# Kernel optimization log

Measured on AMD Instinct MI355X. Metric: run time of the kernel, lower is better.

## Reference

```python
import jax, jax.numpy as jnp
import numpy as np

MARGIN = 0.1
TEMPERATURE = 0.07


def _l2norm(x, eps=1e-12):
    # matches F.normalize(dim=-1): x / max(||x||, eps)
    n = jnp.sqrt(jnp.sum(x * x, axis=-1, keepdims=True))
    return x / jnp.maximum(n, eps)


def setup_inputs() -> dict:
    key = jax.random.key(0)
    k1, k2 = jax.random.split(key)
    N, D = 16384, 512
    return {
        "student_features": jax.random.normal(k1, (N, D), dtype=jnp.float32),
        "teacher_features": jax.random.normal(k2, (N, D), dtype=jnp.float32),
    }


def reference(student_features, teacher_features):
    s = _l2norm(student_features)
    t = _l2norm(teacher_features)
    logits = jnp.matmul(s, t.T) / TEMPERATURE  # [N, N]
    n = logits.shape[0]
    # targets = 2*I - 1 : +1 on diagonal, -1 off-diagonal
    targets = 2.0 * jnp.eye(n, dtype=logits.dtype) - 1.0
    loss = -jnp.sum(jax.nn.log_sigmoid(targets * logits + MARGIN)) / n
    return loss
```

## Files before the change

### kernel.cpp

```cpp
#include <hip/hip_runtime.h>
#include <stdint.h>

#define TEMPERATURE 0.07f
#define MARGIN 0.1f
#define D_DIM 512
#define BM 128
#define BN 256
#define QSCALE 32.0f
#define SCALE_BYTE 0x7A7A7A7A
#define KS_STRIDE 524288


typedef int v8i32 __attribute__((ext_vector_type(8)));
typedef int v4i32 __attribute__((ext_vector_type(4)));
typedef float f32x16 __attribute__((ext_vector_type(16)));

__device__ __forceinline__ float softplus(float x) {
    return fmaxf(x, 0.0f) + __logf(1.0f + __expf(-fabsf(x)));
}

__device__ __forceinline__ unsigned enc_fp4(float v) {
    const float ay = fabsf(v);
    int c = 0;
    c += ay > 0.25f;
    c += ay > 0.75f;
    c += ay > 1.25f;
    c += ay > 1.75f;
    c += ay > 2.5f;
    c += ay > 3.5f;
    c += ay > 5.0f;
    return (unsigned)c | ((__float_as_uint(v) >> 28) & 8u);
}

__global__ __launch_bounds__(256) void norm_quant_pack_kernel(
    const float* __restrict__ s_in, const float* __restrict__ t_in,
    unsigned char* __restrict__ sp, unsigned char* __restrict__ tp,
    float* __restrict__ corr) {
    const int row = blockIdx.x * 4 + (threadIdx.x >> 6);
    const int lane = threadIdx.x & 63;
    const float4* s4 = (const float4*)(s_in + (size_t)row * D_DIM);
    const float4* t4 = (const float4*)(t_in + (size_t)row * D_DIM);
    float4 a0 = s4[lane * 2], a1 = s4[lane * 2 + 1];
    float4 b0 = t4[lane * 2], b1 = t4[lane * 2 + 1];
    float ss = a0.x * a0.x + a0.y * a0.y + a0.z * a0.z + a0.w * a0.w +
               a1.x * a1.x + a1.y * a1.y + a1.z * a1.z + a1.w * a1.w;
    float tt = b0.x * b0.x + b0.y * b0.y + b0.z * b0.z + b0.w * b0.w +
               b1.x * b1.x + b1.y * b1.y + b1.z * b1.z + b1.w * b1.w;
    float st = a0.x * b0.x + a0.y * b0.y + a0.z * b0.z + a0.w * b0.w +
               a1.x * b1.x + a1.y * b1.y + a1.z * b1.z + a1.w * b1.w;
#pragma unroll
    for (int off = 32; off > 0; off >>= 1) {
        ss += __shfl_down(ss, off);
        tt += __shfl_down(tt, off);
        st += __shfl_down(st, off);
    }
    ss = __shfl(ss, 0);
    tt = __shfl(tt, 0);
    const float ns = fmaxf(sqrtf(ss), 1e-12f);
    const float nt = fmaxf(sqrtf(tt), 1e-12f);
    if (lane == 0) {
        const float l = st / (ns * nt) * (1.0f / TEMPERATURE);
        corr[row] = softplus(-l - MARGIN) - softplus(l - MARGIN);
    }
    const float is = QSCALE / ns, it = QSCALE / nt;
    const unsigned ws_ = enc_fp4(a0.x * is) | (enc_fp4(a0.y * is) << 4) |
                         (enc_fp4(a0.z * is) << 8) | (enc_fp4(a0.w * is) << 12) |
                         (enc_fp4(a1.x * is) << 16) | (enc_fp4(a1.y * is) << 20) |
                         (enc_fp4(a1.z * is) << 24) | (enc_fp4(a1.w * is) << 28);
    const unsigned wt_ = enc_fp4(b0.x * it) | (enc_fp4(b0.y * it) << 4) |
                         (enc_fp4(b0.z * it) << 8) | (enc_fp4(b0.w * it) << 12) |
                         (enc_fp4(b1.x * it) << 16) | (enc_fp4(b1.y * it) << 20) |
                         (enc_fp4(b1.z * it) << 24) | (enc_fp4(b1.w * it) << 28);
    const size_t goff = (size_t)(lane >> 3) * KS_STRIDE +
                        (size_t)(row >> 4) * 512 + ((lane >> 2) & 1) * 256 +
                        (row & 15) * 16 + (lane & 3) * 4;
    *(unsigned*)(sp + goff) = ws_;
    *(unsigned*)(tp + goff) = wt_;
}

__global__ __launch_bounds__(256, 2) void gemm_loss_kernel(
    const unsigned char* __restrict__ Sp, const unsigned char* __restrict__ Tp,
    float* __restrict__ partial) {
    __shared__ float wsums[4];

    const int tid = threadIdx.x;
    const int wave = tid >> 6;
    const int lane = tid & 63;
    const int wm = wave >> 1;
    const int wn = wave & 1;

    const int b = blockIdx.x;
    const int xcd = b & 7;
    const int slot = b >> 3;
    const int sidx = slot >> 6;
    const int within = slot & 63;
    const int st_ = sidx * 8 + xcd;
    const int tm = (st_ >> 4) * 16 + (within >> 2);
    const int tn_ = (st_ & 15) * 4 + (within & 3);

    const int fl4 =
        ((lane >> 4) & 1) * 512 + (lane >> 5) * 256 + (lane & 15) * 16;

    const unsigned char* Ab = Sp + (size_t)(tm * 4 + wm * 2) * 1024 + fl4;
    const unsigned char* Bb = Tp + (size_t)(tn_ * 8 + wn * 4) * 1024 + fl4;

    f32x16 acc[2][4];
#pragma unroll
    for (int pa = 0; pa < 2; ++pa)
#pragma unroll
        for (int pb = 0; pb < 4; ++pb)
#pragma unroll
            for (int r = 0; r < 16; ++r) acc[pa][pb][r] = 0.0f;

    v4i32 aF0[2], bF0[4], aF1[2], bF1[4];

    auto load_step = [&](v4i32(&aF)[2], v4i32(&bF)[4], int ks) {
        const size_t ko = (size_t)ks * KS_STRIDE;
#pragma unroll
        for (int pa = 0; pa < 2; ++pa)
            aF[pa] = *(const v4i32*)(Ab + ko + pa * 1024);
#pragma unroll
        for (int pb = 0; pb < 4; ++pb)
            bF[pb] = *(const v4i32*)(Bb + ko + pb * 1024);
    };
    auto mfma_step = [&](v4i32(&aF)[2], v4i32(&bF)[4]) {
        v8i32 aX[2];
#pragma unroll
        for (int pa = 0; pa < 2; ++pa)
            aX[pa] = __builtin_shufflevector(aF[pa], aF[pa], 0, 1, 2, 3, 0, 1,
                                             2, 3);
#pragma unroll
        for (int pb = 0; pb < 4; ++pb) {
            v8i32 bX = __builtin_shufflevector(bF[pb], bF[pb], 0, 1, 2, 3, 0,
                                               1, 2, 3);
#pragma unroll
            for (int pa = 0; pa < 2; ++pa)
                acc[pa][pb] = __builtin_amdgcn_mfma_scale_f32_32x32x64_f8f6f4(
                    aX[pa], bX, acc[pa][pb], 4 , 4 ,
                    0, SCALE_BYTE, 0, SCALE_BYTE);
        }
    };

    load_step(aF0, bF0, 0);
    load_step(aF1, bF1, 1);
#pragma unroll
    for (int ks = 0; ks < 8; ks += 2) {
        mfma_step(aF0, bF0);
        if (ks + 2 < 8) load_step(aF0, bF0, ks + 2);
        mfma_step(aF1, bF1);
        if (ks + 3 < 8) load_step(aF1, bF1, ks + 3);
    }

    const float C1 = (1.0f / TEMPERATURE) * 1.4426950408889634f;
    const float C2 = -MARGIN * 1.4426950408889634f;
    float ysum = 0.0f, asum = 0.0f, lsum = 0.0f;
#pragma unroll
    for (int pa = 0; pa < 2; ++pa)
#pragma unroll
        for (int pb = 0; pb < 4; ++pb) {
            float prod = 1.0f;
#pragma unroll
            for (int r = 0; r < 16; ++r) {
                const float y = fmaf(acc[pa][pb][r], C1, C2);
                ysum += y;
                const float ay = fabsf(y);
                asum += ay;
                prod = fmaf(prod, __builtin_amdgcn_exp2f(-ay), prod);
            }
            lsum += __builtin_amdgcn_logf(prod);
        }
    float total =
        fmaf(ysum + asum, 0.5f, lsum) * 0.6931471805599453f;
#pragma unroll
    for (int off = 32; off > 0; off >>= 1) total += __shfl_down(total, off);
    if (lane == 0) wsums[wave] = total;
    __syncthreads();
    if (tid == 0)
        partial[b] = wsums[0] + wsums[1] + wsums[2] + wsums[3];
}

__global__ __launch_bounds__(1024) void reduce_kernel(
    const float* __restrict__ partial, int nPartials,
    const float* __restrict__ corr, int nCorr, int N,
    float* __restrict__ out) {
    const float4* p4 = (const float4*)partial;
    const float4* c4 = (const float4*)corr;
    float sx = 0.0f, sy = 0.0f, sz = 0.0f, sw = 0.0f;
    for (int i = threadIdx.x; i < nPartials / 4; i += 1024) {
        float4 v = p4[i];
        sx += v.x; sy += v.y; sz += v.z; sw += v.w;
    }
    for (int i = threadIdx.x; i < nCorr / 4; i += 1024) {
        float4 v = c4[i];
        sx += v.x; sy += v.y; sz += v.z; sw += v.w;
    }
    float s = (sx + sy) + (sz + sw);
#pragma unroll
    for (int off = 32; off > 0; off >>= 1) s += __shfl_down(s, off);
    __shared__ float ws[16];
    const int wave = threadIdx.x >> 6;
    const int lane = threadIdx.x & 63;
    if (lane == 0) ws[wave] = s;
    __syncthreads();
    if (threadIdx.x == 0) {
        float t = 0.0f;
#pragma unroll
        for (int w = 0; w < 16; ++w) t += ws[w];
        out[0] = t / (float)N;
    }
}

extern "C" void kernel_launch(void* const* d_in, const int* in_sizes, int n_in,
                              void* d_out, int out_size, void* d_ws, size_t ws_size,
                              hipStream_t stream) {
    (void)n_in; (void)out_size; (void)ws_size;
    const float* s_in = (const float*)d_in[0];
    const float* t_in = (const float*)d_in[1];
    const int N = in_sizes[0] / D_DIM;

    unsigned char* sp = (unsigned char*)d_ws;
    unsigned char* tp = sp + (size_t)N * (D_DIM / 2);
    float* partial = (float*)(tp + (size_t)N * (D_DIM / 2));
    const int nPartials = (N / BM) * (N / BN);
    float* corr = partial + nPartials;

    norm_quant_pack_kernel<<<N / 4, 256, 0, stream>>>(s_in, t_in, sp, tp,
                                                      corr);
    gemm_loss_kernel<<<nPartials, 256, 0, stream>>>(sp, tp, partial);
    reduce_kernel<<<1, 1024, 0, stream>>>(partial, nPartials, corr, N, N,
                                          (float*)d_out);
}
```

Baseline: 182.6 us.

## Fuse final reduction into GEMM via atomics and coalesce packed-operand stores

The separate reduce kernel is removed: each GEMM block atomically adds its partial into one accumulator, and the last block, chosen by a ticket counter, writes the mean. The norm/quant kernel now handles 16 rows per block, stages the packed FP4 words in shared memory so global stores are contiguous, and atomically adds the diagonal correction. The GEMM drops the explicit double-buffered register prefetch in favour of a simple loop, raises the occupancy hint to 3 blocks, and leaves the upper half of the MFMA operands undefined instead of duplicated. The atomics add contention and make the summation order nondeterministic, and removing the manual prefetch may expose more load latency.

Measured after the change: 338.1 us. 85.2% more time.

```diff
diff --git a/kernel.cpp b/kernel.cpp
--- a/kernel.cpp
+++ b/kernel.cpp
@@ -32,12 +32,15 @@
     return (unsigned)c | ((__float_as_uint(v) >> 28) & 8u);
 }
 
-__global__ __launch_bounds__(256) void norm_quant_pack_kernel(
+__global__ __launch_bounds__(1024) void norm_quant_pack_kernel(
     const float* __restrict__ s_in, const float* __restrict__ t_in,
     unsigned char* __restrict__ sp, unsigned char* __restrict__ tp,
-    float* __restrict__ corr) {
-    const int row = blockIdx.x * 4 + (threadIdx.x >> 6);
+    float* __restrict__ accum) {
+    __shared__ unsigned pls[2048];
+    __shared__ float cshr[16];
+    const int wave = threadIdx.x >> 6;
     const int lane = threadIdx.x & 63;
+    const int row = blockIdx.x * 16 + wave;
     const float4* s4 = (const float4*)(s_in + (size_t)row * D_DIM);
     const float4* t4 = (const float4*)(t_in + (size_t)row * D_DIM);
     float4 a0 = s4[lane * 2], a1 = s4[lane * 2 + 1];
@@ -60,7 +63,7 @@
     const float nt = fmaxf(sqrtf(tt), 1e-12f);
     if (lane == 0) {
         const float l = st / (ns * nt) * (1.0f / TEMPERATURE);
-        corr[row] = softplus(-l - MARGIN) - softplus(l - MARGIN);
+        cshr[wave] = softplus(-l - MARGIN) - softplus(l - MARGIN);
     }
     const float is = QSCALE / ns, it = QSCALE / nt;
     const unsigned ws_ = enc_fp4(a0.x * is) | (enc_fp4(a0.y * is) << 4) |
@@ -71,16 +74,29 @@
                          (enc_fp4(b0.z * it) << 8) | (enc_fp4(b0.w * it) << 12) |
                          (enc_fp4(b1.x * it) << 16) | (enc_fp4(b1.y * it) << 20) |
                          (enc_fp4(b1.z * it) << 24) | (enc_fp4(b1.w * it) << 28);
-    const size_t goff = (size_t)(lane >> 3) * KS_STRIDE +
-                        (size_t)(row >> 4) * 512 + ((lane >> 2) & 1) * 256 +
-                        (row & 15) * 16 + (lane & 3) * 4;
-    *(unsigned*)(sp + goff) = ws_;
-    *(unsigned*)(tp + goff) = wt_;
-}
-
-__global__ __launch_bounds__(256, 2) void gemm_loss_kernel(
+    const int widx =
+        (lane >> 3) * 128 + ((lane >> 2) & 1) * 64 + wave * 4 + (lane & 3);
+    pls[widx] = ws_;
+    pls[1024 + widx] = wt_;
+    __syncthreads();
+    const int t = threadIdx.x;
+    const int ks = t >> 7, rem = t & 127;
+    const size_t goff = (size_t)ks * KS_STRIDE + (size_t)blockIdx.x * 512 +
+                        (size_t)rem * 4;
+    *(unsigned*)(sp + goff) = pls[t];
+    *(unsigned*)(tp + goff) = pls[1024 + t];
+    if (t == 0) {
+        float c = 0.0f;
+#pragma unroll
+        for (int w = 0; w < 16; ++w) c += cshr[w];
+        atomicAdd(accum, c);
+    }
+}
+
+__global__ __launch_bounds__(256, 3) void gemm_loss_kernel(
     const unsigned char* __restrict__ Sp, const unsigned char* __restrict__ Tp,
-    float* __restrict__ partial) {
+    float* __restrict__ accum, unsigned* __restrict__ ticket,
+    float* __restrict__ out, float invN) {
     __shared__ float wsums[4];
 
     const int tid = threadIdx.x;
@@ -112,43 +128,31 @@
 #pragma unroll
             for (int r = 0; r < 16; ++r) acc[pa][pb][r] = 0.0f;
 
-    v4i32 aF0[2], bF0[4], aF1[2], bF1[4];
-
-    auto load_step = [&](v4i32(&aF)[2], v4i32(&bF)[4], int ks) {
+#pragma unroll
+    for (int ks = 0; ks < 8; ++ks) {
         const size_t ko = (size_t)ks * KS_STRIDE;
+        v4i32 aF[2], bF[4];
 #pragma unroll
         for (int pa = 0; pa < 2; ++pa)
             aF[pa] = *(const v4i32*)(Ab + ko + pa * 1024);
 #pragma unroll
         for (int pb = 0; pb < 4; ++pb)
             bF[pb] = *(const v4i32*)(Bb + ko + pb * 1024);
-    };
-    auto mfma_step = [&](v4i32(&aF)[2], v4i32(&bF)[4]) {
         v8i32 aX[2];
 #pragma unroll
         for (int pa = 0; pa < 2; ++pa)
-            aX[pa] = __builtin_shufflevector(aF[pa], aF[pa], 0, 1, 2, 3, 0, 1,
-                                             2, 3);
+            aX[pa] = __builtin_shufflevector(aF[pa], aF[pa], 0, 1, 2, 3, -1,
+                                             -1, -1, -1);
 #pragma unroll
         for (int pb = 0; pb < 4; ++pb) {
-            v8i32 bX = __builtin_shufflevector(bF[pb], bF[pb], 0, 1, 2, 3, 0,
-                                               1, 2, 3);
+            v8i32 bX = __builtin_shufflevector(bF[pb], bF[pb], 0, 1, 2, 3, -1,
+                                               -1, -1, -1);
 #pragma unroll
             for (int pa = 0; pa < 2; ++pa)
                 acc[pa][pb] = __builtin_amdgcn_mfma_scale_f32_32x32x64_f8f6f4(
                     aX[pa], bX, acc[pa][pb], 4 , 4 ,
                     0, SCALE_BYTE, 0, SCALE_BYTE);
         }
-    };
-
-    load_step(aF0, bF0, 0);
-    load_step(aF1, bF1, 1);
-#pragma unroll
-    for (int ks = 0; ks < 8; ks += 2) {
-        mfma_step(aF0, bF0);
-        if (ks + 2 < 8) load_step(aF0, bF0, ks + 2);
-        mfma_step(aF1, bF1);
-        if (ks + 3 < 8) load_step(aF1, bF1, ks + 3);
     }
 
     const float C1 = (1.0f / TEMPERATURE) * 1.4426950408889634f;
@@ -175,38 +179,15 @@
     for (int off = 32; off > 0; off >>= 1) total += __shfl_down(total, off);
     if (lane == 0) wsums[wave] = total;
     __syncthreads();
-    if (tid == 0)
-        partial[b] = wsums[0] + wsums[1] + wsums[2] + wsums[3];
-}
-
-__global__ __launch_bounds__(1024) void reduce_kernel(
-    const float* __restrict__ partial, int nPartials,
-    const float* __restrict__ corr, int nCorr, int N,
-    float* __restrict__ out) {
-    const float4* p4 = (const float4*)partial;
-    const float4* c4 = (const float4*)corr;
-    float sx = 0.0f, sy = 0.0f, sz = 0.0f, sw = 0.0f;
-    for (int i = threadIdx.x; i < nPartials / 4; i += 1024) {
-        float4 v = p4[i];
-        sx += v.x; sy += v.y; sz += v.z; sw += v.w;
-    }
-    for (int i = threadIdx.x; i < nCorr / 4; i += 1024) {
-        float4 v = c4[i];
-        sx += v.x; sy += v.y; sz += v.z; sw += v.w;
-    }
-    float s = (sx + sy) + (sz + sw);
-#pragma unroll
-    for (int off = 32; off > 0; off >>= 1) s += __shfl_down(s, off);
-    __shared__ float ws[16];
-    const int wave = threadIdx.x >> 6;
-    const int lane = threadIdx.x & 63;
-    if (lane == 0) ws[wave] = s;
-    __syncthreads();
-    if (threadIdx.x == 0) {
-        float t = 0.0f;
-#pragma unroll
-        for (int w = 0; w < 16; ++w) t += ws[w];
-        out[0] = t / (float)N;
+    if (tid == 0) {
+        const float t = wsums[0] + wsums[1] + wsums[2] + wsums[3];
+        atomicAdd(accum, t);
+        __threadfence();
+        const unsigned got = atomicAdd(ticket, 1u);
+        if (got == gridDim.x - 1) {
+            const float full = atomicAdd(accum, 0.0f);
+            out[0] = full * invN;
+        }
     }
 }
 
@@ -220,13 +201,14 @@
 
     unsigned char* sp = (unsigned char*)d_ws;
     unsigned char* tp = sp + (size_t)N * (D_DIM / 2);
-    float* partial = (float*)(tp + (size_t)N * (D_DIM / 2));
-    const int nPartials = (N / BM) * (N / BN);
-    float* corr = partial + nPartials;
-
-    norm_quant_pack_kernel<<<N / 4, 256, 0, stream>>>(s_in, t_in, sp, tp,
-                                                      corr);
-    gemm_loss_kernel<<<nPartials, 256, 0, stream>>>(sp, tp, partial);
-    reduce_kernel<<<1, 1024, 0, stream>>>(partial, nPartials, corr, N, N,
-                                          (float*)d_out);
-}
+    float* accum = (float*)(tp + (size_t)N * (D_DIM / 2));
+    unsigned* ticket = (unsigned*)(accum + 1);
+    const int nBlocks = (N / BM) * (N / BN);
+
+    hipMemsetAsync(accum, 0, 8, stream);
+    norm_quant_pack_kernel<<<N / 16, 1024, 0, stream>>>(s_in, t_in, sp, tp,
+                                                        accum);
+    gemm_loss_kernel<<<nBlocks, 256, 0, stream>>>(sp, tp, accum, ticket,
+                                                  (float*)d_out,
+                                                  1.0f / (float)N);
+}
```
